# Kernel optimization log

Hardware: AMD Instinct MI355X
Metric: run time of the kernel (lower is better)

The kernel has to match this reference:

```python
import jax, jax.numpy as jnp
import numpy as np

STEP = 0.1  # step_size from init
H = 2048    # ceil(dim/2)


def setup_inputs() -> dict:
    key = jax.random.key(0)
    k1, k2, k3 = jax.random.split(key, 3)
    B, h = 16384, H
    x = jax.random.normal(k1, (B, 2 * h), dtype=jnp.float32)
    # Xavier-uniform-like scale for [2h, h] linear weights
    scale = (6.0 / (h + 2 * h)) ** 0.5
    W0 = jax.random.normal(k2, (2 * h, h), dtype=jnp.float32) * scale
    W1 = jax.random.normal(k3, (2 * h, h), dtype=jnp.float32) * scale
    b0 = jnp.zeros((2 * h,), dtype=jnp.float32)
    b1 = jnp.zeros((2 * h,), dtype=jnp.float32)
    return {"x": x, "W0": W0, "b0": b0, "W1": W1, "b1": b1}


def reference(x, W0, b0, W1, b1):
    h = W0.shape[1]
    u_old = x[:, :h]          # [B, h]
    v_old = x[:, h:]          # [B, h]
    # stage 1: Linear(u) -> tanh -> W1^T matmul -> scaled residual add
    v_mid = jnp.tanh(u_old @ W1.T + b1)   # [B, 2h]
    v_sig = v_mid @ W1                     # [B, h]  (tied-weight transpose matmul)
    v_new = v_old + STEP * v_sig
    # stage 2: Linear(v_new) -> tanh -> W0^T matmul -> scaled residual sub
    u_mid = jnp.tanh(v_new @ W0.T + b0)   # [B, 2h]
    u_sig = u_mid @ W0                     # [B, h]
    u_new = u_old - STEP * u_sig
    return jnp.concatenate((u_new, v_new), axis=1)
```

## Files before the change

kernel.cpp:

```cpp
#include <hip/hip_runtime.h>
#include <hip/hip_bf16.h>
#include <stdint.h>


typedef __attribute__((ext_vector_type(8))) short short8;
typedef __attribute__((ext_vector_type(4))) float f32x4;

#define DEVINL __device__ __forceinline__

DEVINL ushort f2b(float f) {
  union { float f; uint32_t u; } v; v.f = f;
  uint32_t u = v.u;
  return (ushort)((u + 0x7fffu + ((u >> 16) & 1u)) >> 16);
}

DEVINL float fast_tanh(float x) {
  x = fminf(10.0f, fmaxf(-10.0f, x));
  float e = __expf(2.0f * x);
  return (e - 1.0f) * __builtin_amdgcn_rcpf(e + 1.0f);
}

DEVINL void gload16(const ushort* g, ushort* l) {
  __builtin_amdgcn_global_load_lds(
      (const __attribute__((address_space(1))) void*)g,
      (__attribute__((address_space(3))) void*)l, 16, 0, 0);
}

template<int MH, int NH>
DEVINL void mfma_quad(f32x4 (&acc)[8][4], const short8 (&a)[4][2],
                      const short8 (&b)[2][2]) {
#pragma unroll
  for (int ks = 0; ks < 2; ++ks)
#pragma unroll
    for (int mi = 0; mi < 4; ++mi)
#pragma unroll
      for (int ni = 0; ni < 2; ++ni)
        acc[MH * 4 + mi][NH * 2 + ni] = __builtin_amdgcn_mfma_f32_16x16x32_bf16(
            a[mi][ks], b[ni][ks], acc[MH * 4 + mi][NH * 2 + ni], 0, 0, 0);
}

template<int MODE, int SCHED>
__global__ __launch_bounds__(512, 2)
void gemm256(const ushort* __restrict__ A, const ushort* __restrict__ Bt,
             const float* __restrict__ bias, ushort* __restrict__ Tout,
             const float* __restrict__ xres, float* __restrict__ outres,
             ushort* __restrict__ vbout, float step, int M, int N, int K)
{
  __shared__ __align__(16) ushort ldsU[65536];

  const int tid  = threadIdx.x;
  const int wave = tid >> 6, lane = tid & 63;
  const int wr = wave >> 2, wc = wave & 3;
  const int lr = lane & 15, hi = lane >> 4;

  const int GX = gridDim.x;
  const int nwg = GX * gridDim.y;
  const int lin = blockIdx.y * GX + blockIdx.x;
  const int swz = (lin & 7) * (nwg >> 3) + (lin >> 3);
  const int by = swz / GX, bx = swz - by * GX;
  const int m0 = by * 256, n0 = bx * 256;

  const int kb_st = ((tid & 7) * 16) ^ (((tid >> 3) & 7) << 4);
  int offA[2][2], offB[2][2];
#pragma unroll
  for (int j = 0; j < 2; ++j) {
    const int rp = j * 64 + (tid >> 3);
#pragma unroll
    for (int h = 0; h < 2; ++h) {
      offA[h][j] = (m0 + (rp >> 6) * 128 + h * 64 + (rp & 63)) * K + (kb_st >> 1);
      offB[h][j] = (n0 + (rp >> 5) * 64 + h * 32 + (rp & 31)) * K + (kb_st >> 1);
    }
  }

#define STAGE_A(buf, half, t) do {                                             \
    gload16(A + (size_t)offA[half][0] + (size_t)(t) * 64,                      \
            ldsU + (buf) * 32768 + (half) * 8192 + tid * 8);                   \
    gload16(A + (size_t)offA[half][1] + (size_t)(t) * 64,                      \
            ldsU + (buf) * 32768 + (half) * 8192 + 4096 + tid * 8);            \
  } while (0)
#define STAGE_B(buf, half, t) do {                                             \
    gload16(Bt + (size_t)offB[half][0] + (size_t)(t) * 64,                     \
            ldsU + (buf) * 32768 + 16384 + (half) * 8192 + tid * 8);           \
    gload16(Bt + (size_t)offB[half][1] + (size_t)(t) * 64,                     \
            ldsU + (buf) * 32768 + 16384 + (half) * 8192 + 4096 + tid * 8);    \
  } while (0)

  const int xm = (lane & 7) << 4;
  const int kbr0 = (hi * 16) ^ xm;
  const int kbr1 = (64 + hi * 16) ^ xm;
  const int eA0 = (wr * 64 + lr) * 64 + (kbr0 >> 1);
  const int eA1 = (wr * 64 + lr) * 64 + (kbr1 >> 1);
  const int eB0 = (wc * 32 + lr) * 64 + (kbr0 >> 1);
  const int eB1 = (wc * 32 + lr) * 64 + (kbr1 >> 1);

#define LDSE(idx) (*(const short8*)&ldsU[idx])
#define READ_A8(dst, buf, half) do {                                           \
    dst[0][0] = LDSE((buf)*32768 + (half)*8192 +    0 + eA0);                  \
    dst[0][1] = LDSE((buf)*32768 + (half)*8192 +    0 + eA1);                  \
    dst[1][0] = LDSE((buf)*32768 + (half)*8192 + 1024 + eA0);                  \
    dst[1][1] = LDSE((buf)*32768 + (half)*8192 + 1024 + eA1);                  \
    dst[2][0] = LDSE((buf)*32768 + (half)*8192 + 2048 + eA0);                  \
    dst[2][1] = LDSE((buf)*32768 + (half)*8192 + 2048 + eA1);                  \
    dst[3][0] = LDSE((buf)*32768 + (half)*8192 + 3072 + eA0);                  \
    dst[3][1] = LDSE((buf)*32768 + (half)*8192 + 3072 + eA1);                  \
  } while (0)
#define READ_B4(dst, buf, half) do {                                           \
    dst[0][0] = LDSE((buf)*32768 + 16384 + (half)*8192 +    0 + eB0);          \
    dst[0][1] = LDSE((buf)*32768 + 16384 + (half)*8192 +    0 + eB1);          \
    dst[1][0] = LDSE((buf)*32768 + 16384 + (half)*8192 + 1024 + eB0);          \
    dst[1][1] = LDSE((buf)*32768 + 16384 + (half)*8192 + 1024 + eB1);          \
  } while (0)

  f32x4 acc[8][4] = {};
  short8 a0[4][2], a1[4][2], b0[2][2], b1[2][2];

#define VM6 asm volatile("s_waitcnt vmcnt(6)" ::: "memory")
#define VM0 asm volatile("s_waitcnt vmcnt(0)" ::: "memory")
#define PHASE_TAIL(MH, NH, AF, BF)                                             \
  __builtin_amdgcn_s_barrier();                                                \
  asm volatile("s_waitcnt lgkmcnt(0)" ::: "memory");                           \
  __builtin_amdgcn_sched_barrier(0);                                           \
  __builtin_amdgcn_s_setprio(1);                                               \
  mfma_quad<MH, NH>(acc, AF, BF);                                              \
  __builtin_amdgcn_s_setprio(0);                                               \
  __builtin_amdgcn_s_barrier();
#define PHASE_TAIL2(MHa, NHa, AFa, BFa, MHb, NHb, AFb, BFb)                    \
  __builtin_amdgcn_s_barrier();                                                \
  asm volatile("s_waitcnt lgkmcnt(0)" ::: "memory");                           \
  __builtin_amdgcn_sched_barrier(0);                                           \
  __builtin_amdgcn_s_setprio(1);                                               \
  mfma_quad<MHa, NHa>(acc, AFa, BFa);                                          \
  mfma_quad<MHb, NHb>(acc, AFb, BFb);                                          \
  __builtin_amdgcn_s_setprio(0);                                               \
  __builtin_amdgcn_s_barrier();

  const int NT = K >> 6;
  const int NI = NT >> 1;

  STAGE_A(0, 0, 0); STAGE_A(0, 1, 0); STAGE_B(0, 0, 0); STAGE_B(0, 1, 0);
  STAGE_A(1, 0, 1); STAGE_B(1, 0, 1); STAGE_A(1, 1, 1);
  VM6;
  __builtin_amdgcn_s_barrier();

  if constexpr (SCHED == 0) {
#pragma unroll 1
    for (int i = 0; i < NI - 1; ++i) {
      const int t = 2 * i;
      READ_A8(a0, 0, 0); READ_B4(b0, 0, 0);
      STAGE_B(1, 1, t + 1);
      PHASE_TAIL(0, 0, a0, b0)
      READ_A8(a1, 0, 1);
      STAGE_A(0, 0, t + 2);
      PHASE_TAIL(1, 0, a1, b0)
      READ_B4(b1, 0, 1);
      STAGE_A(0, 1, t + 2);
      PHASE_TAIL(0, 1, a0, b1)
      STAGE_B(0, 0, t + 2);
      VM6;
      PHASE_TAIL(1, 1, a1, b1)
      READ_A8(a0, 1, 0); READ_B4(b0, 1, 0);
      STAGE_B(0, 1, t + 2);
      PHASE_TAIL(0, 0, a0, b0)
      READ_A8(a1, 1, 1);
      STAGE_A(1, 0, t + 3);
      PHASE_TAIL(1, 0, a1, b0)
      READ_B4(b1, 1, 1);
      STAGE_A(1, 1, t + 3);
      PHASE_TAIL(0, 1, a0, b1)
      STAGE_B(1, 0, t + 3);
      VM6;
      PHASE_TAIL(1, 1, a1, b1)
    }
    {
      const int t = NT - 2;
      READ_A8(a0, 0, 0); READ_B4(b0, 0, 0);
      STAGE_B(1, 1, t + 1);
      PHASE_TAIL(0, 0, a0, b0)
      READ_A8(a1, 0, 1);
      PHASE_TAIL(1, 0, a1, b0)
      READ_B4(b1, 0, 1);
      PHASE_TAIL(0, 1, a0, b1)
      VM0;
      PHASE_TAIL(1, 1, a1, b1)
      READ_A8(a0, 1, 0); READ_B4(b0, 1, 0);
      PHASE_TAIL(0, 0, a0, b0)
      READ_A8(a1, 1, 1);
      PHASE_TAIL(1, 0, a1, b0)
      READ_B4(b1, 1, 1);
      PHASE_TAIL(0, 1, a0, b1)
      PHASE_TAIL(1, 1, a1, b1)
    }
  } else {
#pragma unroll 1
    for (int i = 0; i < NI - 1; ++i) {
      const int t = 2 * i;
      READ_A8(a0, 0, 0); READ_B4(b0, 0, 0); READ_A8(a1, 0, 1);
      STAGE_B(1, 1, t + 1);
      PHASE_TAIL2(0, 0, a0, b0, 1, 0, a1, b0)
      READ_B4(b1, 0, 1);
      STAGE_A(0, 0, t + 2); STAGE_A(0, 1, t + 2); STAGE_B(0, 0, t + 2);
      VM6;
      PHASE_TAIL2(0, 1, a0, b1, 1, 1, a1, b1)
      READ_A8(a0, 1, 0); READ_B4(b0, 1, 0); READ_A8(a1, 1, 1);
      STAGE_B(0, 1, t + 2);
      PHASE_TAIL2(0, 0, a0, b0, 1, 0, a1, b0)
      READ_B4(b1, 1, 1);
      STAGE_A(1, 0, t + 3); STAGE_A(1, 1, t + 3); STAGE_B(1, 0, t + 3);
      VM6;
      PHASE_TAIL2(0, 1, a0, b1, 1, 1, a1, b1)
    }
    {
      const int t = NT - 2;
      READ_A8(a0, 0, 0); READ_B4(b0, 0, 0); READ_A8(a1, 0, 1);
      STAGE_B(1, 1, t + 1);
      PHASE_TAIL2(0, 0, a0, b0, 1, 0, a1, b0)
      READ_B4(b1, 0, 1);
      VM0;
      PHASE_TAIL2(0, 1, a0, b1, 1, 1, a1, b1)
      READ_A8(a0, 1, 0); READ_B4(b0, 1, 0); READ_A8(a1, 1, 1);
      PHASE_TAIL2(0, 0, a0, b0, 1, 0, a1, b0)
      READ_B4(b1, 1, 1);
      PHASE_TAIL2(0, 1, a0, b1, 1, 1, a1, b1)
    }
  }

  const int mrow0 = m0 + wr * 128 + hi * 4;
  const int ncol0 = n0 + wc * 64 + lr;
#pragma unroll
  for (int mi = 0; mi < 8; ++mi) {
#pragma unroll
    for (int ni = 0; ni < 4; ++ni) {
      const int col = ncol0 + ni * 16;
      if (MODE == 0) {
        const float bv = bias[col];
#pragma unroll
        for (int r = 0; r < 4; ++r) {
          const int row = mrow0 + mi * 16 + r;
          Tout[(size_t)row * N + col] = f2b(fast_tanh(acc[mi][ni][r] + bv));
        }
      } else {
#pragma unroll
        for (int r = 0; r < 4; ++r) {
          const int row = mrow0 + mi * 16 + r;
          const size_t oi = (size_t)row * 4096 + col;
          const float v = fmaf(step, acc[mi][ni][r], xres[oi]);
          outres[oi] = v;
          if (MODE == 1) vbout[(size_t)row * N + col] = f2b(v);
        }
      }
    }
  }
#undef STAGE_A
#undef STAGE_B
#undef LDSE
#undef READ_A8
#undef READ_B4
#undef PHASE_TAIL
#undef PHASE_TAIL2
#undef VM6
#undef VM0
}

__global__ void cast_strided_half(const float* __restrict__ x,
                                  ushort* __restrict__ dst)
{
  const int i = blockIdx.x * blockDim.x + threadIdx.x;
  const int row = i >> 9;
  const int c4  = (i & 511) * 4;
  const float4 v = *(const float4*)&x[(size_t)row * 4096 + c4];
  ushort4 o;
  o.x = f2b(v.x); o.y = f2b(v.y); o.z = f2b(v.z); o.w = f2b(v.w);
  *(ushort4*)&dst[(size_t)row * 2048 + c4] = o;
}

__global__ void pack_w(const float* __restrict__ W,
                       ushort* __restrict__ Wb, ushort* __restrict__ Wt)
{
  __shared__ float tile[32][33];
  const int bx = blockIdx.x * 32;
  const int by = blockIdx.y * 32;
  const int tx = threadIdx.x, ty = threadIdx.y;
#pragma unroll
  for (int j = ty; j < 32; j += 8) {
    const float v = W[(size_t)(by + j) * 2048 + bx + tx];
    tile[j][tx] = v;
    Wb[(size_t)(by + j) * 2048 + bx + tx] = f2b(v);
  }
  __syncthreads();
#pragma unroll
  for (int j = ty; j < 32; j += 8) {
    Wt[(size_t)(bx + j) * 4096 + by + tx] = f2b(tile[tx][j]);
  }
}

extern "C" void kernel_launch(void* const* d_in, const int* in_sizes, int n_in,
                              void* d_out, int out_size, void* d_ws, size_t ws_size,
                              hipStream_t stream)
{
  const float* x  = (const float*)d_in[0];
  const float* W0 = (const float*)d_in[1];
  const float* b0 = (const float*)d_in[2];
  const float* W1 = (const float*)d_in[3];
  const float* b1 = (const float*)d_in[4];
  float* out = (float*)d_out;

  const int Mrows = 16384, H2 = 4096, Hh = 2048;

  uint8_t* ws = (uint8_t*)d_ws;
  ushort* T   = (ushort*)ws;
  ushort* Ab  = (ushort*)(ws + (size_t)134217728);
  ushort* W0b = (ushort*)(ws + (size_t)134217728 + 67108864);
  ushort* W0t = W0b + 8388608;
  ushort* W1b = W0t + 8388608;
  ushort* W1t = W1b + 8388608;

  cast_strided_half<<<32768, 256, 0, stream>>>(x, Ab);
  dim3 pw_grid(64, 128), pw_blk(32, 8);
  pack_w<<<pw_grid, pw_blk, 0, stream>>>(W1, W1b, W1t);
  pack_w<<<pw_grid, pw_blk, 0, stream>>>(W0, W0b, W0t);

  dim3 blk(512);
  dim3 g1(H2 / 256, Mrows / 256);
  dim3 g2(Hh / 256, Mrows / 256);

  gemm256<0, 0><<<g1, blk, 0, stream>>>(Ab, W1b, b1, T,
                                        nullptr, nullptr, nullptr, 0.f,
                                        Mrows, H2, Hh);
  gemm256<1, 0><<<g2, blk, 0, stream>>>(T, W1t, nullptr, nullptr,
                                        x + Hh, out + Hh, Ab, 0.1f,
                                        Mrows, Hh, H2);
  gemm256<0, 1><<<g1, blk, 0, stream>>>(Ab, W0b, b0, T,
                                        nullptr, nullptr, nullptr, 0.f,
                                        Mrows, H2, Hh);
  gemm256<2, 0><<<g2, blk, 0, stream>>>(T, W0t, nullptr, nullptr,
                                        x, out, nullptr, -0.1f,
                                        Mrows, Hh, H2);
}
```

Measured before the change: 1.202 ms.

## Switch GEMMs to two-phase schedule and add simple double-buffer schedule variant

Replaces the fine-grained four-phase MFMA/load interleaving with a two-phase schedule for three of the four GEMMs. Adds a new simple double-buffered schedule that loads the full next tile, waits on all loads, and runs 64 MFMAs per tile; the third GEMM uses it. The aim is to cut barrier count and scheduling overhead, at the risk of exposing global-load latency through full vmcnt(0) waits.

Result: slower. 1.346 ms (+12.0%).

```diff
diff --git a/kernel.cpp b/kernel.cpp
--- a/kernel.cpp
+++ b/kernel.cpp
@@ -110,20 +110,16 @@
     dst[1][0] = LDSE((buf)*32768 + 16384 + (half)*8192 + 1024 + eB0);          \
     dst[1][1] = LDSE((buf)*32768 + 16384 + (half)*8192 + 1024 + eB1);          \
   } while (0)
+#define READ24(buf) do {                                                       \
+    READ_A8(a0, buf, 0); READ_B4(b0, buf, 0);                                  \
+    READ_A8(a1, buf, 1); READ_B4(b1, buf, 1);                                  \
+  } while (0)
 
   f32x4 acc[8][4] = {};
   short8 a0[4][2], a1[4][2], b0[2][2], b1[2][2];
 
 #define VM6 asm volatile("s_waitcnt vmcnt(6)" ::: "memory")
 #define VM0 asm volatile("s_waitcnt vmcnt(0)" ::: "memory")
-#define PHASE_TAIL(MH, NH, AF, BF)                                             \
-  __builtin_amdgcn_s_barrier();                                                \
-  asm volatile("s_waitcnt lgkmcnt(0)" ::: "memory");                           \
-  __builtin_amdgcn_sched_barrier(0);                                           \
-  __builtin_amdgcn_s_setprio(1);                                               \
-  mfma_quad<MH, NH>(acc, AF, BF);                                              \
-  __builtin_amdgcn_s_setprio(0);                                               \
-  __builtin_amdgcn_s_barrier();
 #define PHASE_TAIL2(MHa, NHa, AFa, BFa, MHb, NHb, AFb, BFb)                    \
   __builtin_amdgcn_s_barrier();                                                \
   asm volatile("s_waitcnt lgkmcnt(0)" ::: "memory");                           \
@@ -133,64 +129,25 @@
   mfma_quad<MHb, NHb>(acc, AFb, BFb);                                          \
   __builtin_amdgcn_s_setprio(0);                                               \
   __builtin_amdgcn_s_barrier();
+#define MFMA64 do {                                                            \
+    mfma_quad<0, 0>(acc, a0, b0); mfma_quad<1, 0>(acc, a1, b0);                \
+    mfma_quad<0, 1>(acc, a0, b1); mfma_quad<1, 1>(acc, a1, b1);                \
+  } while (0)
+#define TAIL64                                                                 \
+  asm volatile("s_waitcnt lgkmcnt(0)" ::: "memory");                           \
+  __builtin_amdgcn_sched_barrier(0);                                           \
+  __builtin_amdgcn_s_setprio(1);                                               \
+  MFMA64;                                                                      \
+  __builtin_amdgcn_s_setprio(0);
 
   const int NT = K >> 6;
   const int NI = NT >> 1;
 
-  STAGE_A(0, 0, 0); STAGE_A(0, 1, 0); STAGE_B(0, 0, 0); STAGE_B(0, 1, 0);
-  STAGE_A(1, 0, 1); STAGE_B(1, 0, 1); STAGE_A(1, 1, 1);
-  VM6;
-  __builtin_amdgcn_s_barrier();
-
-  if constexpr (SCHED == 0) {
-#pragma unroll 1
-    for (int i = 0; i < NI - 1; ++i) {
-      const int t = 2 * i;
-      READ_A8(a0, 0, 0); READ_B4(b0, 0, 0);
-      STAGE_B(1, 1, t + 1);
-      PHASE_TAIL(0, 0, a0, b0)
-      READ_A8(a1, 0, 1);
-      STAGE_A(0, 0, t + 2);
-      PHASE_TAIL(1, 0, a1, b0)
-      READ_B4(b1, 0, 1);
-      STAGE_A(0, 1, t + 2);
-      PHASE_TAIL(0, 1, a0, b1)
-      STAGE_B(0, 0, t + 2);
-      VM6;
-      PHASE_TAIL(1, 1, a1, b1)
-      READ_A8(a0, 1, 0); READ_B4(b0, 1, 0);
-      STAGE_B(0, 1, t + 2);
-      PHASE_TAIL(0, 0, a0, b0)
-      READ_A8(a1, 1, 1);
-      STAGE_A(1, 0, t + 3);
-      PHASE_TAIL(1, 0, a1, b0)
-      READ_B4(b1, 1, 1);
-      STAGE_A(1, 1, t + 3);
-      PHASE_TAIL(0, 1, a0, b1)
-      STAGE_B(1, 0, t + 3);
-      VM6;
-      PHASE_TAIL(1, 1, a1, b1)
-    }
-    {
-      const int t = NT - 2;
-      READ_A8(a0, 0, 0); READ_B4(b0, 0, 0);
-      STAGE_B(1, 1, t + 1);
-      PHASE_TAIL(0, 0, a0, b0)
-      READ_A8(a1, 0, 1);
-      PHASE_TAIL(1, 0, a1, b0)
-      READ_B4(b1, 0, 1);
-      PHASE_TAIL(0, 1, a0, b1)
-      VM0;
-      PHASE_TAIL(1, 1, a1, b1)
-      READ_A8(a0, 1, 0); READ_B4(b0, 1, 0);
-      PHASE_TAIL(0, 0, a0, b0)
-      READ_A8(a1, 1, 1);
-      PHASE_TAIL(1, 0, a1, b0)
-      READ_B4(b1, 1, 1);
-      PHASE_TAIL(0, 1, a0, b1)
-      PHASE_TAIL(1, 1, a1, b1)
-    }
-  } else {
+  if constexpr (SCHED == 1) {
+    STAGE_A(0, 0, 0); STAGE_A(0, 1, 0); STAGE_B(0, 0, 0); STAGE_B(0, 1, 0);
+    STAGE_A(1, 0, 1); STAGE_B(1, 0, 1); STAGE_A(1, 1, 1);
+    VM6;
+    __builtin_amdgcn_s_barrier();
 #pragma unroll 1
     for (int i = 0; i < NI - 1; ++i) {
       const int t = 2 * i;
@@ -222,6 +179,37 @@
       READ_B4(b1, 1, 1);
       PHASE_TAIL2(0, 1, a0, b1, 1, 1, a1, b1)
     }
+  } else {
+    STAGE_A(0, 0, 0); STAGE_A(0, 1, 0); STAGE_B(0, 0, 0); STAGE_B(0, 1, 0);
+#pragma unroll 1
+    for (int i = 0; i < NI - 1; ++i) {
+      const int t = 2 * i;
+      VM0;
+      __builtin_amdgcn_s_barrier();
+      READ24(0);
+      STAGE_A(1, 0, t + 1); STAGE_A(1, 1, t + 1);
+      STAGE_B(1, 0, t + 1); STAGE_B(1, 1, t + 1);
+      TAIL64
+      VM0;
+      __builtin_amdgcn_s_barrier();
+      READ24(1);
+      STAGE_A(0, 0, t + 2); STAGE_A(0, 1, t + 2);
+      STAGE_B(0, 0, t + 2); STAGE_B(0, 1, t + 2);
+      TAIL64
+    }
+    {
+      const int t = NT - 2;
+      VM0;
+      __builtin_amdgcn_s_barrier();
+      READ24(0);
+      STAGE_A(1, 0, t + 1); STAGE_A(1, 1, t + 1);
+      STAGE_B(1, 0, t + 1); STAGE_B(1, 1, t + 1);
+      TAIL64
+      VM0;
+      __builtin_amdgcn_s_barrier();
+      READ24(1);
+      TAIL64
+    }
   }
 
   const int mrow0 = m0 + wr * 128 + hi * 4;
@@ -255,8 +243,10 @@
 #undef LDSE
 #undef READ_A8
 #undef READ_B4
-#undef PHASE_TAIL
+#undef READ24
 #undef PHASE_TAIL2
+#undef MFMA64
+#undef TAIL64
 #undef VM6
 #undef VM0
 }
@@ -323,16 +313,16 @@
   dim3 g1(H2 / 256, Mrows / 256);
   dim3 g2(Hh / 256, Mrows / 256);
 
-  gemm256<0, 0><<<g1, blk, 0, stream>>>(Ab, W1b, b1, T,
+  gemm256<0, 1><<<g1, blk, 0, stream>>>(Ab, W1b, b1, T,
                                         nullptr, nullptr, nullptr, 0.f,
                                         Mrows, H2, Hh);
-  gemm256<1, 0><<<g2, blk, 0, stream>>>(T, W1t, nullptr, nullptr,
+  gemm256<1, 1><<<g2, blk, 0, stream>>>(T, W1t, nullptr, nullptr,
                                         x + Hh, out + Hh, Ab, 0.1f,
                                         Mrows, Hh, H2);
-  gemm256<0, 1><<<g1, blk, 0, stream>>>(Ab, W0b, b0, T,
+  gemm256<0, 2><<<g1, blk, 0, stream>>>(Ab, W0b, b0, T,
                                         nullptr, nullptr, nullptr, 0.f,
                                         Mrows, H2, Hh);
-  gemm256<2, 0><<<g2, blk, 0, stream>>>(T, W0t, nullptr, nullptr,
+  gemm256<2, 1><<<g2, blk, 0, stream>>>(T, W0t, nullptr, nullptr,
                                         x, out, nullptr, -0.1f,
                                         Mrows, Hh, H2);
 }
```
